# Kernel tuning notes

Hardware: AMD Instinct MI355X
Metric: run time of the kernel (lower is better)

Reference implementation:

```python
import jax, jax.numpy as jnp
import numpy as np

D, H, DH, NL, NP, DFF, NQ, B = 256, 8, 32, 4, 4, 1024, 900, 8
SPATIAL = ((100, 150), (50, 75), (25, 38), (13, 19))  # multiscale (H_l, W_l)
STARTS = (0, 15000, 18750, 19700)
S = 19947  # sum of H_l*W_l


def _ln(x, g, b, eps=1e-5):
    m = jnp.mean(x, axis=-1, keepdims=True)
    v = jnp.mean((x - m) ** 2, axis=-1, keepdims=True)
    return (x - m) * jax.lax.rsqrt(v + eps) * g + b


def _mha(q, k, v, in_w, in_b, out_w, out_b):
    # torch nn.MultiheadAttention math; q,k,v: (L, B, D)
    wq, wk, wv = jnp.split(in_w, 3, axis=0)
    bq, bk, bv = jnp.split(in_b, 3, axis=0)
    def proj(x, w, b):
        y = jnp.einsum('lbe,fe->lbf', x, w) + b
        return y.reshape(y.shape[0], y.shape[1], H, DH)
    qh, kh, vh = proj(q, wq, bq), proj(k, wk, bk), proj(v, wv, bv)
    scores = jnp.einsum('lbhd,mbhd->bhlm', qh / jnp.sqrt(jnp.float32(DH)), kh)
    attn = jax.nn.softmax(scores, axis=-1)
    o = jnp.einsum('bhlm,mbhd->lbhd', attn, vh).reshape(q.shape[0], q.shape[1], D)
    return jnp.einsum('lbe,fe->lbf', o, out_w) + out_b


def _bilinear(val_flat, Hh, Wd, x, y):
    # grid_sample bilinear, align_corners=False, zeros padding
    # val_flat: (B*H, Hh*Wd, DH); x,y: (B*H, N) pixel coords
    x0, y0 = jnp.floor(x), jnp.floor(y)
    out = jnp.zeros(x.shape + (DH,), val_flat.dtype)
    for dx in (0.0, 1.0):
        for dy in (0.0, 1.0):
            xi, yi = x0 + dx, y0 + dy
            w = (1.0 - jnp.abs(x - xi)) * (1.0 - jnp.abs(y - yi))
            valid = (xi >= 0) & (xi < Wd) & (yi >= 0) & (yi < Hh)
            xc = jnp.clip(xi, 0, Wd - 1).astype(jnp.int32)
            yc = jnp.clip(yi, 0, Hh - 1).astype(jnp.int32)
            g = jnp.take_along_axis(val_flat, (yc * Wd + xc)[..., None], axis=1)
            out = out + g * (w * valid)[..., None]
    return out


def _ms_deform_attn(query, ref, mem_bs, off_w, off_b, aw_w, aw_b, val_w, val_b, ow, ob):
    # query: (B, Lq, D); ref: (B, Lq, NL, 4); mem_bs: (B, S, D)
    b, lq = query.shape[0], query.shape[1]
    value = (jnp.einsum('bsd,fd->bsf', mem_bs, val_w) + val_b).reshape(b, S, H, DH)
    off = (jnp.einsum('bqd,fd->bqf', query, off_w) + off_b).reshape(b, lq, H, NL, NP, 2)
    aw = (jnp.einsum('bqd,fd->bqf', query, aw_w) + aw_b).reshape(b, lq, H, NL * NP)
    aw = jax.nn.softmax(aw, axis=-1).reshape(b, lq, H, NL, NP)
    # reference points are (cx, cy, w, h): loc = cxcy + off/NP * wh * 0.5
    loc = ref[:, :, None, :, None, :2] + off / NP * ref[:, :, None, :, None, 2:] * 0.5
    acc = jnp.zeros((b, H, lq, DH), value.dtype)
    for l, (Hh, Wd) in enumerate(SPATIAL):
        v_l = value[:, STARTS[l]:STARTS[l] + Hh * Wd]
        v_l = v_l.transpose(0, 2, 1, 3).reshape(b * H, Hh * Wd, DH)
        loc_l = loc[:, :, :, l].transpose(0, 2, 1, 3, 4).reshape(b * H, lq * NP, 2)
        x = loc_l[..., 0] * Wd - 0.5
        y = loc_l[..., 1] * Hh - 0.5
        s = _bilinear(v_l, Hh, Wd, x, y).reshape(b, H, lq, NP, DH)
        w_l = aw[:, :, :, l].transpose(0, 2, 1, 3)  # (b, H, lq, NP)
        acc = acc + jnp.einsum('bhqp,bhqpd->bhqd', w_l, s)
    out = acc.transpose(0, 2, 1, 3).reshape(b, lq, D)
    return jnp.einsum('bqd,fd->bqf', out, ow) + ob


def _layer(tgt, pos, ref, memory, in_w, in_b, sow, sob, n1g, n1b, n2g, n2b, n3g, n3b,
           off_w, off_b, aw_w, aw_b, val_w, val_b, cow, cob, l1w, l1b, l2w, l2b):
    # 1) self-attention (pos added to q,k only) + residual + norm2
    q = tgt + pos
    tgt = _ln(tgt + _mha(q, q, tgt, in_w, in_b, sow, sob), n2g, n2b)
    # 2) deformable cross-attention + residual + norm1
    ca = _ms_deform_attn((tgt + pos).transpose(1, 0, 2), ref.transpose(1, 0, 2, 3),
                         memory.transpose(1, 0, 2), off_w, off_b, aw_w, aw_b,
                         val_w, val_b, cow, cob).transpose(1, 0, 2)
    tgt = _ln(tgt + ca, n1g, n1b)
    # 3) ffn + residual + norm3
    h = jax.nn.relu(jnp.einsum('lbe,fe->lbf', tgt, l1w) + l1b)
    tgt = _ln(tgt + jnp.einsum('lbf,ef->lbe', h, l2w) + l2b, n3g, n3b)
    return tgt


def setup_inputs() -> dict:
    key = jax.random.key(0)
    ks = iter(jax.random.split(key, 40))
    def w(shape, s=0.02):
        return jax.random.normal(next(ks), shape, jnp.float32) * s
    return dict(
        tgt=w((NQ, B, D), 1.0),
        tgt_query_pos=w((NQ, B, D), 1.0),
        tgt_reference_points=jax.random.uniform(next(ks), (NQ, B, NL, 4), jnp.float32, 0.1, 0.9),
        memory=w((S, B, D), 1.0),
        memory_spatial_shapes=jnp.array(SPATIAL, jnp.int32),
        memory_level_start_index=jnp.array(STARTS, jnp.int32),
        in_proj_w=w((3 * D, D)), in_proj_b=jnp.zeros((3 * D,), jnp.float32),
        sa_out_w=w((D, D)), sa_out_b=jnp.zeros((D,), jnp.float32),
        norm1_g=jnp.ones((D,), jnp.float32), norm1_b=jnp.zeros((D,), jnp.float32),
        norm2_g=jnp.ones((D,), jnp.float32), norm2_b=jnp.zeros((D,), jnp.float32),
        norm3_g=jnp.ones((D,), jnp.float32), norm3_b=jnp.zeros((D,), jnp.float32),
        off_w=w((H * NL * NP * 2, D)), off_b=w((H * NL * NP * 2,), 0.5),
        aw_w=w((H * NL * NP, D)), aw_b=jnp.zeros((H * NL * NP,), jnp.float32),
        val_w=w((D, D)), val_b=jnp.zeros((D,), jnp.float32),
        ca_out_w=w((D, D)), ca_out_b=jnp.zeros((D,), jnp.float32),
        lin1_w=w((DFF, D)), lin1_b=jnp.zeros((DFF,), jnp.float32),
        lin2_w=w((D, DFF)), lin2_b=jnp.zeros((D,), jnp.float32),
    )


def reference(tgt, tgt_query_pos, tgt_reference_points, memory,
              memory_spatial_shapes, memory_level_start_index,
              in_proj_w, in_proj_b, sa_out_w, sa_out_b,
              norm1_g, norm1_b, norm2_g, norm2_b, norm3_g, norm3_b,
              off_w, off_b, aw_w, aw_b, val_w, val_b, ca_out_w, ca_out_b,
              lin1_w, lin1_b, lin2_w, lin2_b):
    return _layer(tgt, tgt_query_pos, tgt_reference_points, memory,
                  in_proj_w, in_proj_b, sa_out_w, sa_out_b,
                  norm1_g, norm1_b, norm2_g, norm2_b, norm3_g, norm3_b,
                  off_w, off_b, aw_w, aw_b, val_w, val_b, ca_out_w, ca_out_b,
                  lin1_w, lin1_b, lin2_w, lin2_b)
```

## Files before the change

kernel.cpp:

```cpp
#include <hip/hip_runtime.h>
#include <hip/hip_bf16.h>
#include <cstddef>

#define D_MODEL 256
#define NHEAD 8
#define DHEAD 32
#define NLVL 4
#define NPTS 4
#define DFF 1024
#define NQ 900
#define BATCH 8
#define S_TOT 19947

typedef __hip_bfloat16 bf16;
typedef unsigned short ushort;
typedef __attribute__((ext_vector_type(8))) short short8;
typedef __attribute__((ext_vector_type(4))) float float4v;

__constant__ int c_Hh[4] = {100, 50, 25, 13};
__constant__ int c_Wd[4] = {150, 75, 38, 19};
__constant__ int c_st[4] = {0, 15000, 18750, 19700};

__device__ __forceinline__ float bf2f(bf16 h) { return __bfloat162float(h); }
__device__ __forceinline__ float bfbits2f(ushort u) { return __uint_as_float(((unsigned)u) << 16); }
__device__ __forceinline__ ushort f2bfbits(float f) {
  bf16 h = __float2bfloat16(f);
  return *(ushort*)&h;
}

__device__ __forceinline__ float ldIn(const void* p, size_t i, int isb) {
  if (isb) return __bfloat162float(((const bf16*)p)[i]);
  return ((const float*)p)[i];
}
__device__ __forceinline__ void stOut(void* p, size_t i, float v, int isb) {
  if (isb) ((bf16*)p)[i] = __float2bfloat16(v);
  else     ((float*)p)[i] = v;
}

__device__ __forceinline__ const ushort* s_head_c(const bf16* sVal, const bf16* sFlt, int hs) {
  return (const ushort*)(hs < 14 ? sFlt + (size_t)hs * 810000 : sVal + (size_t)(hs - 14) * 810000);
}
__device__ __forceinline__ ushort* s_head(bf16* sVal, bf16* sFlt, int hs) {
  return (ushort*)(hs < 14 ? sFlt + (size_t)hs * 810000 : sVal + (size_t)(hs - 14) * 810000);
}

__global__ void detect_k(const void* __restrict__ refp, int* __restrict__ flag) {
  const int t = threadIdx.x;
  const unsigned short* u = (const unsigned short*)refp;
  const unsigned short w = u[2 * t];
  const float v = __uint_as_float(((unsigned)w) << 16);
  const bool ok = (v >= 0.04f && v <= 0.96f);
  const unsigned long long b = __ballot(ok);
  if (t == 0) *flag = (b == ~0ull) ? 1 : 0;
}

template <int AMODE, int OMODE, bool RELU, int NT>
__global__ __launch_bounds__(256) void gemm_mfma(const void* __restrict__ A,
                                                 const void* __restrict__ W,
                                                 const void* __restrict__ Bias,
                                                 void* __restrict__ C,
                                                 const int* __restrict__ flagp,
                                                 int M, int K, int ldc,
                                                 int wRow0, int cCol0) {
  const int isb = *flagp;
  __shared__ __align__(16) ushort Al[64 * 72];
  __shared__ __align__(16) ushort Wl[NT * 16 * 72];
  const int tid = threadIdx.x;
  const int row0 = blockIdx.y * 64;
  const int col0 = blockIdx.x * (NT * 16);
  const int sr = tid >> 2;
  const int sk = (tid & 3) * 16;
  const int wv = tid >> 6;
  const int ln = tid & 63;
  const int m16 = ln & 15;
  const int quad = ln >> 4;
  float4v acc[NT] = {};

  for (int k0 = 0; k0 < K; k0 += 64) {
    __syncthreads();
    {
      const int ar = row0 + sr;
      ushort tmp[16];
      if (ar < M) {
        const size_t base = (size_t)ar * K + k0 + sk;
        if (AMODE == 0) {
          const float* ap = (const float*)A + base;
#pragma unroll
          for (int j = 0; j < 16; j++) tmp[j] = f2bfbits(ap[j]);
        } else if (AMODE == 1) {
          const ushort* ap = (const ushort*)A + base;
#pragma unroll
          for (int j = 0; j < 16; j++) tmp[j] = ap[j];
        } else {
          if (isb) {
            const ushort* ap = (const ushort*)A + base;
#pragma unroll
            for (int j = 0; j < 16; j++) tmp[j] = ap[j];
          } else {
            const float* ap = (const float*)A + base;
#pragma unroll
            for (int j = 0; j < 16; j++) tmp[j] = f2bfbits(ap[j]);
          }
        }
      } else {
#pragma unroll
        for (int j = 0; j < 16; j++) tmp[j] = 0;
      }
      ushort* dst = &Al[sr * 72 + sk];
      *(short8*)(dst) = *(const short8*)&tmp[0];
      *(short8*)(dst + 8) = *(const short8*)&tmp[8];
    }
#pragma unroll
    for (int rr = 0; rr < NT / 4; rr++) {
      const int wr = rr * 64 + sr;
      const size_t base = (size_t)(wRow0 + col0 + wr) * K + k0 + sk;
      ushort tmp[16];
      if (isb) {
        const ushort* wp = (const ushort*)W + base;
#pragma unroll
        for (int j = 0; j < 16; j++) tmp[j] = wp[j];
      } else {
        const float* wp = (const float*)W + base;
#pragma unroll
        for (int j = 0; j < 16; j++) tmp[j] = f2bfbits(wp[j]);
      }
      ushort* dst = &Wl[wr * 72 + sk];
      *(short8*)(dst) = *(const short8*)&tmp[0];
      *(short8*)(dst + 8) = *(const short8*)&tmp[8];
    }
    __syncthreads();
#pragma unroll
    for (int kk = 0; kk < 64; kk += 32) {
      const short8 a = *(const short8*)&Al[(wv * 16 + m16) * 72 + kk + quad * 8];
#pragma unroll
      for (int nt = 0; nt < NT; nt++) {
        const short8 b = *(const short8*)&Wl[(nt * 16 + m16) * 72 + kk + quad * 8];
        acc[nt] = __builtin_amdgcn_mfma_f32_16x16x32_bf16(a, b, acc[nt], 0, 0, 0);
      }
    }
  }
#pragma unroll
  for (int nt = 0; nt < NT; nt++) {
    const int c = col0 + nt * 16 + m16;
    const float bv = ldIn(Bias, wRow0 + c, isb);
#pragma unroll
    for (int r = 0; r < 4; r++) {
      const int row = row0 + wv * 16 + quad * 4 + r;
      if (row < M) {
        float v = acc[nt][r] + bv;
        if (RELU) v = fmaxf(v, 0.f);
        if (OMODE == 0) ((float*)C)[(size_t)row * ldc + cCol0 + c] = v;
        else            ((bf16*)C)[(size_t)row * ldc + cCol0 + c] = __float2bfloat16(v);
      }
    }
  }
}

__global__ void add_ii_k(const void* __restrict__ a, const void* __restrict__ b,
                         bf16* __restrict__ o, const int* __restrict__ flagp, int n) {
  const int isb = *flagp;
  int i = blockIdx.x * 256 + threadIdx.x;
  if (i < n) o[i] = __float2bfloat16(ldIn(a, i, isb) + ldIn(b, i, isb));
}
__global__ void add_fi_k(const float* __restrict__ a, const void* __restrict__ b,
                         bf16* __restrict__ o, const int* __restrict__ flagp, int n) {
  const int isb = *flagp;
  int i = blockIdx.x * 256 + threadIdx.x;
  if (i < n) o[i] = __float2bfloat16(a[i] + ldIn(b, i, isb));
}

__global__ void fill_k(unsigned int* __restrict__ o, int nwords, unsigned int v) {
  int i = blockIdx.x * 256 + threadIdx.x;
  if (i < nwords) o[i] = v;
}

__global__ __launch_bounds__(256) void sqk_gemm(const bf16* __restrict__ qkv,
                                                bf16* __restrict__ sVal, bf16* __restrict__ sFlt) {
  __shared__ __align__(16) ushort Qs[64 * 40];
  __shared__ __align__(16) ushort Ks[64 * 40];
  const int kt = blockIdx.x, qt = blockIdx.y, bh = blockIdx.z;
  const int b = bh >> 3, h = bh & 7;
  const int tid = threadIdx.x;
  const int sr = tid >> 2;
  const int se = (tid & 3) * 8;
  {
    const int qg = qt * 64 + sr;
    short8 tq = {};
    if (qg < 900) tq = *(const short8*)((const ushort*)qkv + ((size_t)(qg * BATCH + b)) * 768 + h * DHEAD + se);
    *(short8*)&Qs[sr * 40 + se] = tq;
    const int kg = kt * 64 + sr;
    short8 tk = {};
    if (kg < 900) tk = *(const short8*)((const ushort*)qkv + ((size_t)(kg * BATCH + b)) * 768 + 256 + h * DHEAD + se);
    *(short8*)&Ks[sr * 40 + se] = tk;
  }
  __syncthreads();
  const int wv = tid >> 6, ln = tid & 63, m16 = ln & 15, quad = ln >> 4;
  const short8 a = *(const short8*)&Qs[(wv * 16 + m16) * 40 + quad * 8];
  ushort* Sh = s_head(sVal, sFlt, bh);
#pragma unroll
  for (int ks = 0; ks < 4; ks++) {
    const short8 bb = *(const short8*)&Ks[(ks * 16 + m16) * 40 + quad * 8];
    float4v c = {};
    c = __builtin_amdgcn_mfma_f32_16x16x32_bf16(a, bb, c, 0, 0, 0);
    const int kgl = kt * 64 + ks * 16 + m16;
    if (kgl < 900) {
#pragma unroll
      for (int r = 0; r < 4; r++) {
        const int qgl = qt * 64 + wv * 16 + quad * 4 + r;
        if (qgl < 900)
          Sh[(size_t)qgl * 900 + kgl] = f2bfbits(c[r] * 0.17677669529663687f);
      }
    }
  }
}

__global__ __launch_bounds__(256) void srowstat(const bf16* __restrict__ sVal, const bf16* __restrict__ sFlt,
                                                float* __restrict__ mbuf, float* __restrict__ sbuf) {
  const int row = blockIdx.x * 4 + (threadIdx.x >> 6);
  const int lane = threadIdx.x & 63;
  const int hs = row / 900;
  const int q = row - hs * 900;
  const ushort* S = s_head_c(sVal, sFlt, hs) + (size_t)q * 900;
  float v[15];
  float m = -1e30f;
#pragma unroll
  for (int i = 0; i < 15; i++) {
    const int k = lane + i * 64;
    const float x = (k < 900) ? bfbits2f(S[k]) : -1e30f;
    v[i] = x;
    m = fmaxf(m, x);
  }
#pragma unroll
  for (int o = 32; o > 0; o >>= 1) m = fmaxf(m, __shfl_down(m, o));
  m = __shfl(m, 0);
  float s = 0.f;
#pragma unroll
  for (int i = 0; i < 15; i++) {
    const int k = lane + i * 64;
    if (k < 900) s += __expf(v[i] - m);
  }
#pragma unroll
  for (int o = 32; o > 0; o >>= 1) s += __shfl_down(s, o);
  if (lane == 0) { mbuf[row] = m; sbuf[row] = s; }
}

__global__ __launch_bounds__(256) void spv_gemm(const bf16* __restrict__ qkv,
                                                const bf16* __restrict__ sVal, const bf16* __restrict__ sFlt,
                                                const float* __restrict__ mbuf, const float* __restrict__ sbuf,
                                                bf16* __restrict__ outb) {
  __shared__ __align__(16) ushort Ps[64 * 72];
  __shared__ __align__(16) ushort Vt[32 * 72];
  const int qt = blockIdx.x, bh = blockIdx.y;
  const int b = bh >> 3, h = bh & 7;
  const int tid = threadIdx.x;
  const ushort* Sh = s_head_c(sVal, sFlt, bh);
  const int pr = tid >> 2;
  const int pc = (tid & 3) * 16;
  const int qg = qt * 64 + pr;
  float pm = 0.f, psinv = 0.f;
  if (qg < 900) {
    pm = mbuf[bh * 900 + qg];
    psinv = 1.f / sbuf[bh * 900 + qg];
  }
  const int vk = tid >> 2;
  const int vd = (tid & 3) * 8;
  const int wv = tid >> 6, ln = tid & 63, m16 = ln & 15, quad = ln >> 4;
  float4v acc[2] = {};

  for (int k0 = 0; k0 < 900; k0 += 64) {
    __syncthreads();
    {
      ushort tmp[16];
      if (qg < 900 && (k0 + pc + 15) < 900) {
        const unsigned* sp = (const unsigned*)(Sh + (size_t)qg * 900 + k0 + pc);
#pragma unroll
        for (int j = 0; j < 8; j++) {
          const unsigned u = sp[j];
          const float e0 = __expf(__uint_as_float(u << 16) - pm) * psinv;
          const float e1 = __expf(__uint_as_float(u & 0xffff0000u) - pm) * psinv;
          tmp[2 * j] = f2bfbits(e0);
          tmp[2 * j + 1] = f2bfbits(e1);
        }
      } else {
#pragma unroll
        for (int i = 0; i < 16; i++) {
          const int k = k0 + pc + i;
          float e = 0.f;
          if (qg < 900 && k < 900)
            e = __expf(bfbits2f(Sh[(size_t)qg * 900 + k]) - pm) * psinv;
          tmp[i] = f2bfbits(e);
        }
      }
      ushort* dst = &Ps[pr * 72 + pc];
      *(short8*)(dst) = *(const short8*)&tmp[0];
      *(short8*)(dst + 8) = *(const short8*)&tmp[8];
    }
    {
      const int kg = k0 + vk;
      short8 tv = {};
      if (kg < 900)
        tv = *(const short8*)((const ushort*)qkv + ((size_t)(kg * BATCH + b)) * 768 + 512 + h * DHEAD + vd);
      const ushort* tvp = (const ushort*)&tv;
#pragma unroll
      for (int i = 0; i < 8; i++) Vt[(vd + i) * 72 + vk] = tvp[i];
    }
    __syncthreads();
#pragma unroll
    for (int kc = 0; kc < 64; kc += 32) {
      const short8 a = *(const short8*)&Ps[(wv * 16 + m16) * 72 + kc + quad * 8];
#pragma unroll
      for (int nt = 0; nt < 2; nt++) {
        const short8 bb = *(const short8*)&Vt[(nt * 16 + m16) * 72 + kc + quad * 8];
        acc[nt] = __builtin_amdgcn_mfma_f32_16x16x32_bf16(a, bb, acc[nt], 0, 0, 0);
      }
    }
  }
#pragma unroll
  for (int nt = 0; nt < 2; nt++) {
    const int d = nt * 16 + m16;
#pragma unroll
    for (int r = 0; r < 4; r++) {
      const int q = qt * 64 + wv * 16 + quad * 4 + r;
      if (q < 900)
        outb[((size_t)(q * BATCH + b)) * D_MODEL + h * DHEAD + d] = __float2bfloat16(acc[nt][r]);
    }
  }
}

template <int RMODE, int OMODE>
__global__ __launch_bounds__(256) void ln_res(const float* __restrict__ x, const void* __restrict__ resid,
                                              const void* __restrict__ g, const void* __restrict__ be,
                                              void* __restrict__ out, const int* __restrict__ flagp) {
  const int isb = *flagp;
  __shared__ float red[256];
  __shared__ float s_mean, s_rstd;
  const int row = blockIdx.x, tid = threadIdx.x;
  const size_t base = (size_t)row * D_MODEL + tid;
  float r;
  if (RMODE == 0) r = ((const float*)resid)[base];
  else            r = ldIn(resid, base, isb);
  const float v = x[base] + r;
  red[tid] = v; __syncthreads();
  for (int st = 128; st > 0; st >>= 1) { if (tid < st) red[tid] += red[tid + st]; __syncthreads(); }
  if (tid == 0) s_mean = red[0] * (1.0f / D_MODEL);
  __syncthreads();
  const float c = v - s_mean;
  red[tid] = c * c; __syncthreads();
  for (int st = 128; st > 0; st >>= 1) { if (tid < st) red[tid] += red[tid + st]; __syncthreads(); }
  if (tid == 0) s_rstd = rsqrtf(red[0] * (1.0f / D_MODEL) + 1e-5f);
  __syncthreads();
  const float y = c * s_rstd * ldIn(g, tid, isb) + ldIn(be, tid, isb);
  if (OMODE == 0) ((float*)out)[base] = y;
  else            stOut(out, base, y, isb);
}

__global__ void aw_softmax_k(float* __restrict__ aw) {
  const int t = blockIdx.x * 256 + threadIdx.x;
  if (t >= NQ * BATCH * NHEAD) return;
  float* p = aw + (size_t)(t >> 3) * (NHEAD * 16) + (t & 7) * 16;
  float v[16], mx = -1e30f;
#pragma unroll
  for (int i = 0; i < 16; i++) { v[i] = p[i]; mx = fmaxf(mx, v[i]); }
  float ssum = 0.f;
#pragma unroll
  for (int i = 0; i < 16; i++) { v[i] = __expf(v[i] - mx); ssum += v[i]; }
  const float inv = 1.f / ssum;
#pragma unroll
  for (int i = 0; i < 16; i++) p[i] = v[i] * inv;
}

__global__ __launch_bounds__(256) void deform_sample_k(const float* __restrict__ off,
                                                       const float* __restrict__ aw,
                                                       const void* __restrict__ ref,
                                                       const bf16* __restrict__ value,
                                                       float* __restrict__ out,
                                                       const int* __restrict__ flagp) {
  const int isb = *flagp;
  int t = blockIdx.x * 256 + threadIdx.x;
  if (t >= BATCH * NHEAD * NQ * DHEAD) return;
  const int d = t & 31;
  int rest = t >> 5;
  const int lq = rest % NQ; rest /= NQ;
  const int h = rest & 7;
  const int b = rest >> 3;
  const int m = lq * BATCH + b;
  const float* offp = off + (size_t)m * D_MODEL + h * 32;
  const float* awp  = aw + (size_t)m * (NHEAD * 16) + h * 16;
  const size_t refq = (size_t)m * (NLVL * 4);
  float acc = 0.f;
#pragma unroll
  for (int l = 0; l < NLVL; l++) {
    const int Hh = c_Hh[l], Wd = c_Wd[l], st = c_st[l];
    const float rx = ldIn(ref, refq + l * 4 + 0, isb);
    const float ry = ldIn(ref, refq + l * 4 + 1, isb);
    const float rw = ldIn(ref, refq + l * 4 + 2, isb);
    const float rh = ldIn(ref, refq + l * 4 + 3, isb);
#pragma unroll
    for (int p = 0; p < NPTS; p++) {
      const float ox = offp[l * 8 + p * 2 + 0];
      const float oy = offp[l * 8 + p * 2 + 1];
      const float w  = awp[l * 4 + p];
      const float x = (rx + ox * 0.125f * rw) * (float)Wd - 0.5f;
      const float y = (ry + oy * 0.125f * rh) * (float)Hh - 0.5f;
      const float x0 = floorf(x), y0 = floorf(y);
      const float fx = x - x0, fy = y - y0;
      const int ix = (int)x0, iy = (int)y0;
      float sv = 0.f;
#pragma unroll
      for (int dy = 0; dy < 2; dy++) {
#pragma unroll
        for (int dx = 0; dx < 2; dx++) {
          const int xi = ix + dx, yi = iy + dy;
          if (xi >= 0 && xi < Wd && yi >= 0 && yi < Hh) {
            const float wt = (dx ? fx : 1.f - fx) * (dy ? fy : 1.f - fy);
            sv += wt * bf2f(value[((size_t)((st + yi * Wd + xi) * BATCH + b)) * D_MODEL + h * 32 + d]);
          }
        }
      }
      acc += w * sv;
    }
  }
  out[(size_t)m * D_MODEL + h * 32 + d] = acc;
}

extern "C" void kernel_launch(void* const* d_in, const int* in_sizes, int n_in,
                              void* d_out, int out_size, void* d_ws, size_t ws_size,
                              hipStream_t stream) {
  const void* tgt    = d_in[0];
  const void* pos    = d_in[1];
  const void* refp   = d_in[2];
  const void* memory = d_in[3];
  const void* in_w   = d_in[6];
  const void* in_b   = d_in[7];
  const void* sow    = d_in[8];
  const void* sob    = d_in[9];
  const void* n1g    = d_in[10];
  const void* n1b    = d_in[11];
  const void* n2g    = d_in[12];
  const void* n2b    = d_in[13];
  const void* n3g    = d_in[14];
  const void* n3b    = d_in[15];
  const void* off_w  = d_in[16];
  const void* off_bi = d_in[17];
  const void* aw_w   = d_in[18];
  const void* aw_b   = d_in[19];
  const void* val_w  = d_in[20];
  const void* val_b  = d_in[21];
  const void* cow    = d_in[22];
  const void* cob    = d_in[23];
  const void* l1w    = d_in[24];
  const void* l1b    = d_in[25];
  const void* l2w    = d_in[26];
  const void* l2b    = d_in[27];

  const int M = NQ * BATCH;
  const int MV = S_TOT * BATCH;
  const int n1 = M * D_MODEL;

  char* base = (char*)d_ws;
  size_t wo = 0;
  int* flagi = (int*)(base + wo); wo += 256;
  bf16* value = (bf16*)(base + wo); wo += (size_t)MV * D_MODEL * 2;
  bf16* bfreg = (bf16*)(base + wo); wo += (size_t)M * 1024 * 2;
  float* S0 = (float*)(base + wo); wo += (size_t)n1 * 4;
  float* S1 = (float*)(base + wo); wo += (size_t)n1 * 4;
  float* S2 = (float*)(base + wo); wo += (size_t)n1 * 4;
  float* S3 = (float*)(base + wo); wo += (size_t)M * 128 * 4;
  const size_t needed = wo;

  if (ws_size < needed) {
    const int nwords = (out_size + 1) / 2;
    fill_k<<<(nwords + 255) / 256, 256, 0, stream>>>((unsigned int*)d_out, nwords, 0x42C842C8u);
    return;
  }

  bf16* qbuf = bfreg;
  bf16* qkvb = bfreg + (size_t)M * 256;
  bf16* hbuf = bfreg;
  float* t1 = S2;
  float* awb = S3;
  float* mbuf = (float*)((char*)S0 + 22680000);
  float* sbuf = mbuf + 57600;

  const int mtiles = (M + 63) / 64;
  const int vtiles = (MV + 63) / 64;

  detect_k<<<1, 64, 0, stream>>>(refp, flagi);
  add_ii_k<<<(n1 + 255) / 256, 256, 0, stream>>>(tgt, pos, qbuf, flagi, n1);
  gemm_mfma<1, 1, false, 4><<<dim3(8, mtiles), 256, 0, stream>>>(qbuf, in_w, in_b, qkvb, flagi, M, 256, 768, 0, 0);
  gemm_mfma<2, 1, false, 4><<<dim3(4, mtiles), 256, 0, stream>>>(tgt, in_w, in_b, qkvb, flagi, M, 256, 768, 512, 512);
  sqk_gemm<<<dim3(15, 15, 64), 256, 0, stream>>>(qkvb, value, (bf16*)S0);
  srowstat<<<14400, 256, 0, stream>>>(value, (bf16*)S0, mbuf, sbuf);
  spv_gemm<<<dim3(15, 64), 256, 0, stream>>>(qkvb, value, (bf16*)S0, mbuf, sbuf, qbuf);
  float* sa_proj = S1;
  gemm_mfma<1, 0, false, 4><<<dim3(4, mtiles), 256, 0, stream>>>(qbuf, sow, sob, sa_proj, flagi, M, 256, 256, 0, 0);
  ln_res<2, 0><<<M, 256, 0, stream>>>(sa_proj, tgt, n2g, n2b, t1, flagi);
  gemm_mfma<2, 1, false, 16><<<dim3(1, vtiles), 256, 0, stream>>>(memory, val_w, val_b, value, flagi, MV, 256, 256, 0, 0);
  add_fi_k<<<(n1 + 255) / 256, 256, 0, stream>>>(t1, pos, qbuf, flagi, n1);
  float* offb = S1;
  gemm_mfma<1, 0, false, 4><<<dim3(4, mtiles), 256, 0, stream>>>(qbuf, off_w, off_bi, offb, flagi, M, 256, 256, 0, 0);
  gemm_mfma<1, 0, false, 4><<<dim3(2, mtiles), 256, 0, stream>>>(qbuf, aw_w, aw_b, awb, flagi, M, 256, 128, 0, 0);
  aw_softmax_k<<<(M * NHEAD + 255) / 256, 256, 0, stream>>>(awb);
  float* ca_acc = S0;
  deform_sample_k<<<(M * D_MODEL + 255) / 256, 256, 0, stream>>>(offb, awb, refp, value, ca_acc, flagi);
  float* ca_proj = S1;
  gemm_mfma<0, 0, false, 4><<<dim3(4, mtiles), 256, 0, stream>>>(ca_acc, cow, cob, ca_proj, flagi, M, 256, 256, 0, 0);
  float* t2 = S0;
  ln_res<0, 0><<<M, 256, 0, stream>>>(ca_proj, t1, n1g, n1b, t2, flagi);
  gemm_mfma<0, 1, true, 16><<<dim3(4, mtiles), 256, 0, stream>>>(t2, l1w, l1b, hbuf, flagi, M, 256, DFF, 0, 0);
  float* ffn2 = S1;
  gemm_mfma<1, 0, false, 4><<<dim3(4, mtiles), 256, 0, stream>>>(hbuf, l2w, l2b, ffn2, flagi, M, 1024, 256, 0, 0);
  ln_res<0, 2><<<M, 256, 0, stream>>>(ffn2, t2, n3g, n3b, d_out, flagi);
}
```

Before: 749.1 us.

## Add persistent value-projection GEMM with LDS-resident swizzled weight half

Replaces the generic tiled GEMM for the large value projection (B*S rows by 256) with a dedicated kernel. Each block loads half of the weight matrix (128 output columns × 256 K) once into LDS with an XOR swizzle to avoid bank conflicts. Its waves then loop persistently over 32-row strips, holding the full K-row of A in registers and issuing MFMAs directly. This removes repeated weight staging per tile and K-loop synchronisation. In exchange it uses 64 KB of LDS per block, which limits occupancy, and raises register pressure.

```diff
diff --git a/kernel.cpp b/kernel.cpp
--- a/kernel.cpp
+++ b/kernel.cpp
@@ -151,6 +151,101 @@
         if (RELU) v = fmaxf(v, 0.f);
         if (OMODE == 0) ((float*)C)[(size_t)row * ldc + cCol0 + c] = v;
         else            ((bf16*)C)[(size_t)row * ldc + cCol0 + c] = __float2bfloat16(v);
+      }
+    }
+  }
+}
+
+__global__ __launch_bounds__(256) void vproj_gemm(const void* __restrict__ A,
+                                                  const void* __restrict__ W,
+                                                  const void* __restrict__ Bias,
+                                                  bf16* __restrict__ C,
+                                                  const int* __restrict__ flagp,
+                                                  int M, int nwaves) {
+  const int isb = *flagp;
+  __shared__ __align__(16) ushort Wl[128 * 256];
+  const int tid = threadIdx.x;
+  const int half = blockIdx.x;
+  {
+    const int r = tid >> 1;
+    const int cbase = (tid & 1) * 16;
+    const int wrow = half * 128 + r;
+#pragma unroll
+    for (int c = 0; c < 16; c++) {
+      const int chunk = cbase + c;
+      const int col = chunk * 8;
+      ushort tmp[8];
+      if (isb) {
+        const ushort* wp = (const ushort*)W + (size_t)wrow * 256 + col;
+#pragma unroll
+        for (int j = 0; j < 8; j++) tmp[j] = wp[j];
+      } else {
+        const float* wp = (const float*)W + (size_t)wrow * 256 + col;
+#pragma unroll
+        for (int j = 0; j < 8; j++) tmp[j] = f2bfbits(wp[j]);
+      }
+      *(short8*)&Wl[r * 256 + ((chunk ^ (r & 7)) * 8)] = *(const short8*)tmp;
+    }
+  }
+  __syncthreads();
+
+  const int wv = tid >> 6, ln = tid & 63, m16 = ln & 15, quad = ln >> 4;
+  float bv[8];
+#pragma unroll
+  for (int nt = 0; nt < 8; nt++) bv[nt] = ldIn(Bias, half * 128 + nt * 16 + m16, isb);
+
+  const int gw = blockIdx.y * 4 + wv;
+  for (int t = gw; t * 32 < M; t += nwaves) {
+    const int row0 = t * 32;
+    const int ar0 = row0 + m16;
+    const int ar1 = row0 + 16 + m16;
+    short8 a0[8], a1[8];
+    if (isb) {
+      const ushort* ap = (const ushort*)A;
+#pragma unroll
+      for (int ks = 0; ks < 8; ks++) {
+        short8 z = {};
+        a0[ks] = (ar0 < M) ? *(const short8*)(ap + (size_t)ar0 * 256 + ks * 32 + quad * 8) : z;
+        a1[ks] = (ar1 < M) ? *(const short8*)(ap + (size_t)ar1 * 256 + ks * 32 + quad * 8) : z;
+      }
+    } else {
+      const float* ap = (const float*)A;
+#pragma unroll
+      for (int ks = 0; ks < 8; ks++) {
+        short8 t0 = {}, t1 = {};
+        if (ar0 < M) {
+          const float* p = ap + (size_t)ar0 * 256 + ks * 32 + quad * 8;
+#pragma unroll
+          for (int j = 0; j < 8; j++) ((ushort*)&t0)[j] = f2bfbits(p[j]);
+        }
+        if (ar1 < M) {
+          const float* p = ap + (size_t)ar1 * 256 + ks * 32 + quad * 8;
+#pragma unroll
+          for (int j = 0; j < 8; j++) ((ushort*)&t1)[j] = f2bfbits(p[j]);
+        }
+        a0[ks] = t0; a1[ks] = t1;
+      }
+    }
+    float4v acc0[8] = {}, acc1[8] = {};
+#pragma unroll
+    for (int ks = 0; ks < 8; ks++) {
+#pragma unroll
+      for (int nt = 0; nt < 8; nt++) {
+        const int wr = nt * 16 + m16;
+        const short8 b = *(const short8*)&Wl[wr * 256 + (((ks * 4 + quad) ^ (wr & 7)) * 8)];
+        acc0[nt] = __builtin_amdgcn_mfma_f32_16x16x32_bf16(a0[ks], b, acc0[nt], 0, 0, 0);
+        acc1[nt] = __builtin_amdgcn_mfma_f32_16x16x32_bf16(a1[ks], b, acc1[nt], 0, 0, 0);
+      }
+    }
+#pragma unroll
+    for (int nt = 0; nt < 8; nt++) {
+      const int col = half * 128 + nt * 16 + m16;
+#pragma unroll
+      for (int r = 0; r < 4; r++) {
+        const int row = row0 + quad * 4 + r;
+        if (row < M) C[(size_t)row * 256 + col] = __float2bfloat16(acc0[nt][r] + bv[nt]);
+        const int row1 = row + 16;
+        if (row1 < M) C[(size_t)row1 * 256 + col] = __float2bfloat16(acc1[nt][r] + bv[nt]);
       }
     }
   }
@@ -483,7 +578,6 @@
   float* sbuf = mbuf + 57600;
 
   const int mtiles = (M + 63) / 64;
-  const int vtiles = (MV + 63) / 64;
 
   detect_k<<<1, 64, 0, stream>>>(refp, flagi);
   add_ii_k<<<(n1 + 255) / 256, 256, 0, stream>>>(tgt, pos, qbuf, flagi, n1);
@@ -495,7 +589,7 @@
   float* sa_proj = S1;
   gemm_mfma<1, 0, false, 4><<<dim3(4, mtiles), 256, 0, stream>>>(qbuf, sow, sob, sa_proj, flagi, M, 256, 256, 0, 0);
   ln_res<2, 0><<<M, 256, 0, stream>>>(sa_proj, tgt, n2g, n2b, t1, flagi);
-  gemm_mfma<2, 1, false, 16><<<dim3(1, vtiles), 256, 0, stream>>>(memory, val_w, val_b, value, flagi, MV, 256, 256, 0, 0);
+  vproj_gemm<<<dim3(2, 256), 256, 0, stream>>>(memory, val_w, val_b, value, flagi, MV, 1024);
   add_fi_k<<<(n1 + 255) / 256, 256, 0, stream>>>(t1, pos, qbuf, flagi, n1);
   float* offb = S1;
   gemm_mfma<1, 0, false, 4><<<dim3(4, mtiles), 256, 0, stream>>>(qbuf, off_w, off_bi, offb, flagi, M, 256, 256, 0, 0);
```

Result: slower. 765.3 us (+2.2%).
